# Optimization experiments

Measured on AMD Instinct MI355X. Metric: run time of the kernel, lower is better.

Reference implementation:

```python
import jax, jax.numpy as jnp
import numpy as np

WINDOW = 5
PAD = WINDOW // 2


def _extract_patches(x):
    # x: (B,C,H,W) -> patches (B,C,K*K,H,W) with reflect padding, matching
    # F.pad(mode='reflect') + F.unfold(window, padding=0).
    B, C, H, W = x.shape
    xp = jnp.pad(x, ((0, 0), (0, 0), (PAD, PAD), (PAD, PAD)), mode='reflect')
    patches = jnp.stack(
        [xp[:, :, i:i + H, j:j + W] for i in range(WINDOW) for j in range(WINDOW)],
        axis=2,
    )
    return patches


def setup_inputs() -> dict:
    key = jax.random.key(0)
    k1, k2, k3 = jax.random.split(key, 3)
    x = jax.random.normal(k1, (4, 32, 256, 256), dtype=jnp.float32)
    mix = jax.random.normal(k2, (1, 32, 1, 1), dtype=jnp.float32)
    beta_raw = jax.random.normal(k3, (), dtype=jnp.float32)
    return {"x": x, "mix": mix, "beta_raw": beta_raw}


def reference(x, mix, beta_raw):
    patches = _extract_patches(x)  # (B,C,25,H,W)

    # Max filter (= max_pool2d over reflect-padded input, stride 1)
    max_out = jnp.max(patches, axis=2)

    # Soft (differentiable) median filter
    beta = 5.0 + 45.0 * jax.nn.sigmoid(beta_raw)
    center = jnp.mean(patches, axis=2, keepdims=True)
    weights = jax.nn.softmax(-beta * jnp.abs(patches - center), axis=2)
    median_out = jnp.sum(weights * patches, axis=2)

    lambda_c = jax.nn.sigmoid(mix)  # (1,C,1,1)
    return lambda_c * median_out + (1.0 - lambda_c) * max_out
```

## Files before the change

### kernel.cpp

```cpp
#include <hip/hip_runtime.h>
#include <math.h>

#define HW 256
#define LW 68
#define WLH 12
#define NT 4

typedef float f32x2 __attribute__((ext_vector_type(2)));

__device__ __forceinline__ int reflect_idx(int i) {
    i = (i < 0) ? -i : i;
    i = (i >= HW) ? (2 * HW - 2 - i) : i;
    return i;
}

__device__ __forceinline__ float4 max4(float4 a, float4 b) {
    float4 r; r.x = fmaxf(a.x, b.x); r.y = fmaxf(a.y, b.y);
    r.z = fmaxf(a.z, b.z); r.w = fmaxf(a.w, b.w); return r;
}
__device__ __forceinline__ float4 max34(float4 a, float4 b, float4 c) {
    float4 r; r.x = fmaxf(fmaxf(a.x, b.x), c.x); r.y = fmaxf(fmaxf(a.y, b.y), c.y);
    r.z = fmaxf(fmaxf(a.z, b.z), c.z); r.w = fmaxf(fmaxf(a.w, b.w), c.w); return r;
}
__device__ __forceinline__ float4 add4(float4 a, float4 b) {
    float4 r; r.x = a.x + b.x; r.y = a.y + b.y;
    r.z = a.z + b.z; r.w = a.w + b.w; return r;
}
__device__ __forceinline__ float4 sub4(float4 a, float4 b) {
    float4 r; r.x = a.x - b.x; r.y = a.y - b.y;
    r.z = a.z - b.z; r.w = a.w - b.w; return r;
}

struct Stage {
    float m[WLH];
    float h;
};

__device__ __forceinline__ void proc_row(
    float4 A0, float4 B0, float4 A1, float4 B1, float4 A2, float4 B2,
    float4 A3, float4 B3, float4 A4, float4 B4,
    float4 cmA, float4 cmB, float4 csA, float4 csB,
    float bp, float c04b, float inv_bp, float lam,
    float* __restrict__ orow)
{
    const float cs[8] = {csA.x,csA.y,csA.z,csA.w, csB.x,csB.y,csB.z,csB.w};
    const float cm[8] = {cmA.x,cmA.y,cmA.z,cmA.w, cmB.x,cmB.y,cmB.z,cmB.w};
    const float vv[5][8] = {
        {A0.x,A0.y,A0.z,A0.w, B0.x,B0.y,B0.z,B0.w},
        {A1.x,A1.y,A1.z,A1.w, B1.x,B1.y,B1.z,B1.w},
        {A2.x,A2.y,A2.z,A2.w, B2.x,B2.y,B2.z,B2.w},
        {A3.x,A3.y,A3.z,A3.w, B3.x,B3.y,B3.z,B3.w},
        {A4.x,A4.y,A4.z,A4.w, B4.x,B4.y,B4.z,B4.w}};

    const float t12 = cs[1] + cs[2];
    const float t34 = cs[3] + cs[4];
    const float t56 = cs[5] + cs[6];
    const float u   = t12 + t34;
    const float w_  = t34 + t56;
    const float S[4] = {cs[0] + u, u + cs[5], cs[2] + w_, w_ + cs[7]};

    const float h12 = fmaxf(cm[1], cm[2]);
    const float h34 = fmaxf(cm[3], cm[4]);
    const float h56 = fmaxf(cm[5], cm[6]);
    const float m[4] = {fmaxf(fmaxf(cm[0], h12), h34),
                        fmaxf(fmaxf(h12, h34), cm[5]),
                        fmaxf(fmaxf(cm[2], h34), h56),
                        fmaxf(fmaxf(h34, h56), cm[7])};

    const f32x2 bp2   = {bp, bp};
    const f32x2 nbm01 = {-(S[0] * c04b), -(S[1] * c04b)};
    const f32x2 nbm23 = {-(S[2] * c04b), -(S[3] * c04b)};
    f32x2 ws01 = {0.0f, 0.0f}, ws23 = {0.0f, 0.0f};
    f32x2 wa01 = {0.0f, 0.0f}, wa23 = {0.0f, 0.0f};

    #pragma unroll
    for (int k = 0; k < 5; ++k) {
        #pragma unroll
        for (int j = 0; j < 5; ++j) {
            const f32x2 v01 = {vv[k][j],     vv[k][j + 1]};
            const f32x2 v23 = {vv[k][j + 2], vv[k][j + 3]};
            const f32x2 tv01 = __builtin_elementwise_fma(bp2, v01, nbm01);
            const f32x2 tv23 = __builtin_elementwise_fma(bp2, v23, nbm23);
            f32x2 e01, e23;
            e01.x = __builtin_amdgcn_exp2f(-fabsf(tv01.x));
            e01.y = __builtin_amdgcn_exp2f(-fabsf(tv01.y));
            e23.x = __builtin_amdgcn_exp2f(-fabsf(tv23.x));
            e23.y = __builtin_amdgcn_exp2f(-fabsf(tv23.y));
            ws01 += e01;
            ws23 += e23;
            wa01 = __builtin_elementwise_fma(e01, tv01, wa01);
            wa23 = __builtin_elementwise_fma(e23, tv23, wa23);
        }
    }

    const float ws[4] = {ws01.x, ws01.y, ws23.x, ws23.y};
    const float wa[4] = {wa01.x, wa01.y, wa23.x, wa23.y};

    float o[4];
    #pragma unroll
    for (int p = 0; p < 4; ++p) {
        const float mean = S[p] * 0.04f;
        const float med  = fmaf(wa[p] * __builtin_amdgcn_rcpf(ws[p]), inv_bp, mean);
        o[p] = fmaf(lam, med - m[p], m[p]);
    }
    float4 o4; o4.x = o[0]; o4.y = o[1]; o4.z = o[2]; o4.w = o[3];
    *(float4*)orow = o4;
}

__global__ __launch_bounds__(64)
void maxmedian_kernel(const float* __restrict__ x,
                      const float* __restrict__ mix,
                      const float* __restrict__ beta_raw,
                      float* __restrict__ out,
                      int C) {
    __shared__ __align__(16) float lds[2][WLH * LW];

    const int lane = threadIdx.x;

    const int band  = blockIdx.x;
    const int plane = band >> 5;
    const int by0   = (band & 31) << 3;

    const float* __restrict__ xp = x + (size_t)plane * (HW * HW);

    int gy[WLH];
    #pragma unroll
    for (int k = 0; k < WLH; ++k) gy[k] = reflect_idx(by0 - 2 + k) * HW;

    const int hj   = lane & 3;
    const int hcol = (hj < 2) ? hj : (64 + hj);
    const int hoff = hcol - 2;
    const int gyh  = reflect_idx(by0 - 2 + (lane >> 2)) * HW;

    const int ch = plane % C;
    const float lam  = 1.0f / (1.0f + __expf(-mix[ch]));
    const float beta = 5.0f + 45.0f / (1.0f + __expf(-beta_raw[0]));
    const float bp     = beta * 1.44269504088896f;
    const float inv_bp = 1.0f / bp;
    const float c04b   = 0.04f * bp;

    const int tx = lane & 15;
    const int r0 = (lane >> 4) * 2;

    auto stage_load = [&](int t, Stage& s) {
        const int c0 = t * 64;
        #pragma unroll
        for (int k = 0; k < WLH; ++k)
            s.m[k] = xp[gy[k] + c0 + lane];
        if (lane < 48)
            s.h = xp[gyh + reflect_idx(c0 + hoff)];
    };
    auto stage_write = [&](int buf, const Stage& s) {
        float* __restrict__ b = lds[buf];
        #pragma unroll
        for (int k = 0; k < WLH; ++k)
            b[k * LW + 2 + lane] = s.m[k];
        if (lane < 48)
            b[(lane >> 2) * LW + hcol] = s.h;
    };
    auto compute = [&](int t, int buf) {
        const float* lbase = &lds[buf][r0 * LW + 4 * tx];

        float4 w0a = *(const float4*)(lbase + 0 * LW);
        float4 w0b = *(const float4*)(lbase + 0 * LW + 4);
        float4 w1a = *(const float4*)(lbase + 1 * LW);
        float4 w1b = *(const float4*)(lbase + 1 * LW + 4);
        float4 w2a = *(const float4*)(lbase + 2 * LW);
        float4 w2b = *(const float4*)(lbase + 2 * LW + 4);
        float4 w3a = *(const float4*)(lbase + 3 * LW);
        float4 w3b = *(const float4*)(lbase + 3 * LW + 4);
        float4 w4a = *(const float4*)(lbase + 4 * LW);
        float4 w4b = *(const float4*)(lbase + 4 * LW + 4);
        float4 w5a = *(const float4*)(lbase + 5 * LW);
        float4 w5b = *(const float4*)(lbase + 5 * LW + 4);

        float4 csA = add4(add4(add4(w0a, w1a), add4(w2a, w3a)), w4a);
        float4 csB = add4(add4(add4(w0b, w1b), add4(w2b, w3b)), w4b);

        const float4 p12a = max4(w1a, w2a), p12b = max4(w1b, w2b);
        const float4 p34a = max4(w3a, w4a), p34b = max4(w3b, w4b);
        const float4 cm0a = max34(w0a, p12a, p34a);
        const float4 cm0b = max34(w0b, p12b, p34b);

        float* __restrict__ orow =
            out + (size_t)plane * (HW * HW) + (size_t)(by0 + r0) * HW + (t * 64 + 4 * tx);

        proc_row(w0a,w0b, w1a,w1b, w2a,w2b, w3a,w3b, w4a,w4b,
                 cm0a, cm0b, csA, csB, bp, c04b, inv_bp, lam, orow);

        csA = add4(csA, sub4(w5a, w0a));
        csB = add4(csB, sub4(w5b, w0b));
        const float4 cm1a = max34(p12a, p34a, w5a);
        const float4 cm1b = max34(p12b, p34b, w5b);

        proc_row(w1a,w1b, w2a,w2b, w3a,w3b, w4a,w4b, w5a,w5b,
                 cm1a, cm1b, csA, csB, bp, c04b, inv_bp, lam, orow + HW);
    };

    Stage s0, s1, s2, s3;
    stage_load(0, s0);
    stage_write(0, s0);
    __builtin_amdgcn_wave_barrier();

    stage_load(1, s1);
    compute(0, 0);
    stage_write(1, s1);
    __builtin_amdgcn_wave_barrier();

    stage_load(2, s2);
    compute(1, 1);
    stage_write(0, s2);
    __builtin_amdgcn_wave_barrier();

    stage_load(3, s3);
    compute(2, 0);
    stage_write(1, s3);
    __builtin_amdgcn_wave_barrier();

    compute(3, 1);
}

extern "C" void kernel_launch(void* const* d_in, const int* in_sizes, int n_in,
                              void* d_out, int out_size, void* d_ws, size_t ws_size,
                              hipStream_t stream) {
    const float* x        = (const float*)d_in[0];
    const float* mix      = (const float*)d_in[1];
    const float* beta_raw = (const float*)d_in[2];
    float* out            = (float*)d_out;

    const int planes = in_sizes[0] / (HW * HW);
    const int C      = in_sizes[1];
    const int grid = planes * 32;

    maxmedian_kernel<<<grid, 64, 0, stream>>>(x, mix, beta_raw, out, C);
}
```

Measured before the change: 36.76 us.

## Halve rows per block, double grid, and swizzle block-to-band mapping

Each 64-thread block now handles a 4-row band instead of 8. Every thread computes one output row instead of two, so the grid doubles and the LDS tile shrinks from 12 to 8 rows. The block index is permuted so that consecutive blocks land on different XCD-strided bands, and launch bounds request 4 waves per EU. The aim is more parallelism, lower register pressure and higher occupancy. The cost is more halo reloading (8 rows loaded for 4 output rows instead of 12 for 8) and losing the sliding-window reuse of column sums and maxes between two rows.

```diff
diff --git a/kernel.cpp b/kernel.cpp
--- a/kernel.cpp
+++ b/kernel.cpp
@@ -3,7 +3,7 @@
 
 #define HW 256
 #define LW 68
-#define WLH 12
+#define WLH 8
 #define NT 4
 
 typedef float f32x2 __attribute__((ext_vector_type(2)));
@@ -26,88 +26,13 @@
     float4 r; r.x = a.x + b.x; r.y = a.y + b.y;
     r.z = a.z + b.z; r.w = a.w + b.w; return r;
 }
-__device__ __forceinline__ float4 sub4(float4 a, float4 b) {
-    float4 r; r.x = a.x - b.x; r.y = a.y - b.y;
-    r.z = a.z - b.z; r.w = a.w - b.w; return r;
-}
 
 struct Stage {
     float m[WLH];
     float h;
 };
 
-__device__ __forceinline__ void proc_row(
-    float4 A0, float4 B0, float4 A1, float4 B1, float4 A2, float4 B2,
-    float4 A3, float4 B3, float4 A4, float4 B4,
-    float4 cmA, float4 cmB, float4 csA, float4 csB,
-    float bp, float c04b, float inv_bp, float lam,
-    float* __restrict__ orow)
-{
-    const float cs[8] = {csA.x,csA.y,csA.z,csA.w, csB.x,csB.y,csB.z,csB.w};
-    const float cm[8] = {cmA.x,cmA.y,cmA.z,cmA.w, cmB.x,cmB.y,cmB.z,cmB.w};
-    const float vv[5][8] = {
-        {A0.x,A0.y,A0.z,A0.w, B0.x,B0.y,B0.z,B0.w},
-        {A1.x,A1.y,A1.z,A1.w, B1.x,B1.y,B1.z,B1.w},
-        {A2.x,A2.y,A2.z,A2.w, B2.x,B2.y,B2.z,B2.w},
-        {A3.x,A3.y,A3.z,A3.w, B3.x,B3.y,B3.z,B3.w},
-        {A4.x,A4.y,A4.z,A4.w, B4.x,B4.y,B4.z,B4.w}};
-
-    const float t12 = cs[1] + cs[2];
-    const float t34 = cs[3] + cs[4];
-    const float t56 = cs[5] + cs[6];
-    const float u   = t12 + t34;
-    const float w_  = t34 + t56;
-    const float S[4] = {cs[0] + u, u + cs[5], cs[2] + w_, w_ + cs[7]};
-
-    const float h12 = fmaxf(cm[1], cm[2]);
-    const float h34 = fmaxf(cm[3], cm[4]);
-    const float h56 = fmaxf(cm[5], cm[6]);
-    const float m[4] = {fmaxf(fmaxf(cm[0], h12), h34),
-                        fmaxf(fmaxf(h12, h34), cm[5]),
-                        fmaxf(fmaxf(cm[2], h34), h56),
-                        fmaxf(fmaxf(h34, h56), cm[7])};
-
-    const f32x2 bp2   = {bp, bp};
-    const f32x2 nbm01 = {-(S[0] * c04b), -(S[1] * c04b)};
-    const f32x2 nbm23 = {-(S[2] * c04b), -(S[3] * c04b)};
-    f32x2 ws01 = {0.0f, 0.0f}, ws23 = {0.0f, 0.0f};
-    f32x2 wa01 = {0.0f, 0.0f}, wa23 = {0.0f, 0.0f};
-
-    #pragma unroll
-    for (int k = 0; k < 5; ++k) {
-        #pragma unroll
-        for (int j = 0; j < 5; ++j) {
-            const f32x2 v01 = {vv[k][j],     vv[k][j + 1]};
-            const f32x2 v23 = {vv[k][j + 2], vv[k][j + 3]};
-            const f32x2 tv01 = __builtin_elementwise_fma(bp2, v01, nbm01);
-            const f32x2 tv23 = __builtin_elementwise_fma(bp2, v23, nbm23);
-            f32x2 e01, e23;
-            e01.x = __builtin_amdgcn_exp2f(-fabsf(tv01.x));
-            e01.y = __builtin_amdgcn_exp2f(-fabsf(tv01.y));
-            e23.x = __builtin_amdgcn_exp2f(-fabsf(tv23.x));
-            e23.y = __builtin_amdgcn_exp2f(-fabsf(tv23.y));
-            ws01 += e01;
-            ws23 += e23;
-            wa01 = __builtin_elementwise_fma(e01, tv01, wa01);
-            wa23 = __builtin_elementwise_fma(e23, tv23, wa23);
-        }
-    }
-
-    const float ws[4] = {ws01.x, ws01.y, ws23.x, ws23.y};
-    const float wa[4] = {wa01.x, wa01.y, wa23.x, wa23.y};
-
-    float o[4];
-    #pragma unroll
-    for (int p = 0; p < 4; ++p) {
-        const float mean = S[p] * 0.04f;
-        const float med  = fmaf(wa[p] * __builtin_amdgcn_rcpf(ws[p]), inv_bp, mean);
-        o[p] = fmaf(lam, med - m[p], m[p]);
-    }
-    float4 o4; o4.x = o[0]; o4.y = o[1]; o4.z = o[2]; o4.w = o[3];
-    *(float4*)orow = o4;
-}
-
-__global__ __launch_bounds__(64)
+__global__ __launch_bounds__(64, 4)
 void maxmedian_kernel(const float* __restrict__ x,
                       const float* __restrict__ mix,
                       const float* __restrict__ beta_raw,
@@ -117,9 +42,11 @@
 
     const int lane = threadIdx.x;
 
-    const int band  = blockIdx.x;
-    const int plane = band >> 5;
-    const int by0   = (band & 31) << 3;
+    const int cpx  = gridDim.x >> 3;
+    const int band = (blockIdx.x & 7) * cpx + (blockIdx.x >> 3);
+
+    const int plane = band >> 6;
+    const int by0   = (band & 63) << 2;
 
     const float* __restrict__ xp = x + (size_t)plane * (HW * HW);
 
@@ -140,14 +67,14 @@
     const float c04b   = 0.04f * bp;
 
     const int tx = lane & 15;
-    const int r0 = (lane >> 4) * 2;
+    const int ry = lane >> 4;
 
     auto stage_load = [&](int t, Stage& s) {
         const int c0 = t * 64;
         #pragma unroll
         for (int k = 0; k < WLH; ++k)
             s.m[k] = xp[gy[k] + c0 + lane];
-        if (lane < 48)
+        if (lane < 32)
             s.h = xp[gyh + reflect_idx(c0 + hoff)];
     };
     auto stage_write = [&](int buf, const Stage& s) {
@@ -155,46 +82,93 @@
         #pragma unroll
         for (int k = 0; k < WLH; ++k)
             b[k * LW + 2 + lane] = s.m[k];
-        if (lane < 48)
+        if (lane < 32)
             b[(lane >> 2) * LW + hcol] = s.h;
     };
     auto compute = [&](int t, int buf) {
-        const float* lbase = &lds[buf][r0 * LW + 4 * tx];
-
-        float4 w0a = *(const float4*)(lbase + 0 * LW);
-        float4 w0b = *(const float4*)(lbase + 0 * LW + 4);
-        float4 w1a = *(const float4*)(lbase + 1 * LW);
-        float4 w1b = *(const float4*)(lbase + 1 * LW + 4);
-        float4 w2a = *(const float4*)(lbase + 2 * LW);
-        float4 w2b = *(const float4*)(lbase + 2 * LW + 4);
-        float4 w3a = *(const float4*)(lbase + 3 * LW);
-        float4 w3b = *(const float4*)(lbase + 3 * LW + 4);
-        float4 w4a = *(const float4*)(lbase + 4 * LW);
-        float4 w4b = *(const float4*)(lbase + 4 * LW + 4);
-        float4 w5a = *(const float4*)(lbase + 5 * LW);
-        float4 w5b = *(const float4*)(lbase + 5 * LW + 4);
-
-        float4 csA = add4(add4(add4(w0a, w1a), add4(w2a, w3a)), w4a);
-        float4 csB = add4(add4(add4(w0b, w1b), add4(w2b, w3b)), w4b);
-
-        const float4 p12a = max4(w1a, w2a), p12b = max4(w1b, w2b);
-        const float4 p34a = max4(w3a, w4a), p34b = max4(w3b, w4b);
-        const float4 cm0a = max34(w0a, p12a, p34a);
-        const float4 cm0b = max34(w0b, p12b, p34b);
+        const float* lbase = &lds[buf][ry * LW + 4 * tx];
+
+        const float4 w0a = *(const float4*)(lbase + 0 * LW);
+        const float4 w0b = *(const float4*)(lbase + 0 * LW + 4);
+        const float4 w1a = *(const float4*)(lbase + 1 * LW);
+        const float4 w1b = *(const float4*)(lbase + 1 * LW + 4);
+        const float4 w2a = *(const float4*)(lbase + 2 * LW);
+        const float4 w2b = *(const float4*)(lbase + 2 * LW + 4);
+        const float4 w3a = *(const float4*)(lbase + 3 * LW);
+        const float4 w3b = *(const float4*)(lbase + 3 * LW + 4);
+        const float4 w4a = *(const float4*)(lbase + 4 * LW);
+        const float4 w4b = *(const float4*)(lbase + 4 * LW + 4);
+
+        const float4 csA = add4(add4(add4(w0a, w1a), add4(w2a, w3a)), w4a);
+        const float4 csB = add4(add4(add4(w0b, w1b), add4(w2b, w3b)), w4b);
+        const float4 cmA = max4(max34(w0a, w1a, w2a), max4(w3a, w4a));
+        const float4 cmB = max4(max34(w0b, w1b, w2b), max4(w3b, w4b));
+
+        const float cs[8] = {csA.x,csA.y,csA.z,csA.w, csB.x,csB.y,csB.z,csB.w};
+        const float cm[8] = {cmA.x,cmA.y,cmA.z,cmA.w, cmB.x,cmB.y,cmB.z,cmB.w};
+        const float vv[5][8] = {
+            {w0a.x,w0a.y,w0a.z,w0a.w, w0b.x,w0b.y,w0b.z,w0b.w},
+            {w1a.x,w1a.y,w1a.z,w1a.w, w1b.x,w1b.y,w1b.z,w1b.w},
+            {w2a.x,w2a.y,w2a.z,w2a.w, w2b.x,w2b.y,w2b.z,w2b.w},
+            {w3a.x,w3a.y,w3a.z,w3a.w, w3b.x,w3b.y,w3b.z,w3b.w},
+            {w4a.x,w4a.y,w4a.z,w4a.w, w4b.x,w4b.y,w4b.z,w4b.w}};
+
+        const float t12 = cs[1] + cs[2];
+        const float t34 = cs[3] + cs[4];
+        const float t56 = cs[5] + cs[6];
+        const float u   = t12 + t34;
+        const float w_  = t34 + t56;
+        const float S[4] = {cs[0] + u, u + cs[5], cs[2] + w_, w_ + cs[7]};
+
+        const float h12 = fmaxf(cm[1], cm[2]);
+        const float h34 = fmaxf(cm[3], cm[4]);
+        const float h56 = fmaxf(cm[5], cm[6]);
+        const float m[4] = {fmaxf(fmaxf(cm[0], h12), h34),
+                            fmaxf(fmaxf(h12, h34), cm[5]),
+                            fmaxf(fmaxf(cm[2], h34), h56),
+                            fmaxf(fmaxf(h34, h56), cm[7])};
+
+        const f32x2 bp2   = {bp, bp};
+        const f32x2 nbm01 = {-(S[0] * c04b), -(S[1] * c04b)};
+        const f32x2 nbm23 = {-(S[2] * c04b), -(S[3] * c04b)};
+        f32x2 ws01 = {0.0f, 0.0f}, ws23 = {0.0f, 0.0f};
+        f32x2 wa01 = {0.0f, 0.0f}, wa23 = {0.0f, 0.0f};
+
+        #pragma unroll
+        for (int k = 0; k < 5; ++k) {
+            #pragma unroll
+            for (int j = 0; j < 5; ++j) {
+                const f32x2 v01 = {vv[k][j],     vv[k][j + 1]};
+                const f32x2 v23 = {vv[k][j + 2], vv[k][j + 3]};
+                const f32x2 tv01 = __builtin_elementwise_fma(bp2, v01, nbm01);
+                const f32x2 tv23 = __builtin_elementwise_fma(bp2, v23, nbm23);
+                f32x2 e01, e23;
+                e01.x = __builtin_amdgcn_exp2f(-fabsf(tv01.x));
+                e01.y = __builtin_amdgcn_exp2f(-fabsf(tv01.y));
+                e23.x = __builtin_amdgcn_exp2f(-fabsf(tv23.x));
+                e23.y = __builtin_amdgcn_exp2f(-fabsf(tv23.y));
+                ws01 += e01;
+                ws23 += e23;
+                wa01 = __builtin_elementwise_fma(e01, tv01, wa01);
+                wa23 = __builtin_elementwise_fma(e23, tv23, wa23);
+            }
+        }
+
+        const float ws[4] = {ws01.x, ws01.y, ws23.x, ws23.y};
+        const float wa[4] = {wa01.x, wa01.y, wa23.x, wa23.y};
+
+        float o[4];
+        #pragma unroll
+        for (int p = 0; p < 4; ++p) {
+            const float mean = S[p] * 0.04f;
+            const float med  = fmaf(wa[p] * __builtin_amdgcn_rcpf(ws[p]), inv_bp, mean);
+            o[p] = fmaf(lam, med - m[p], m[p]);
+        }
+        float4 o4; o4.x = o[0]; o4.y = o[1]; o4.z = o[2]; o4.w = o[3];
 
         float* __restrict__ orow =
-            out + (size_t)plane * (HW * HW) + (size_t)(by0 + r0) * HW + (t * 64 + 4 * tx);
-
-        proc_row(w0a,w0b, w1a,w1b, w2a,w2b, w3a,w3b, w4a,w4b,
-                 cm0a, cm0b, csA, csB, bp, c04b, inv_bp, lam, orow);
-
-        csA = add4(csA, sub4(w5a, w0a));
-        csB = add4(csB, sub4(w5b, w0b));
-        const float4 cm1a = max34(p12a, p34a, w5a);
-        const float4 cm1b = max34(p12b, p34b, w5b);
-
-        proc_row(w1a,w1b, w2a,w2b, w3a,w3b, w4a,w4b, w5a,w5b,
-                 cm1a, cm1b, csA, csB, bp, c04b, inv_bp, lam, orow + HW);
+            out + (size_t)plane * (HW * HW) + (size_t)(by0 + ry) * HW + (t * 64 + 4 * tx);
+        *(float4*)orow = o4;
     };
 
     Stage s0, s1, s2, s3;
@@ -230,7 +204,7 @@
 
     const int planes = in_sizes[0] / (HW * HW);
     const int C      = in_sizes[1];
-    const int grid = planes * 32;
+    const int grid = planes * 64;
 
     maxmedian_kernel<<<grid, 64, 0, stream>>>(x, mix, beta_raw, out, C);
 }
```

Result: slower. 39.52 us (+7.5%).
